# Kernel tuning notes

Hardware: AMD Instinct MI355X
Metric: run time of the kernel (lower is better)

## Reference

```python
import jax, jax.numpy as jnp
import numpy as np

EPS = 1e-12  # F.normalize default eps


def _sage_conv(x, src, dst, num_nodes, W_l, W_r, b):
    # mean-aggregate neighbor features: for each dst node, mean over x[src]
    agg = jax.ops.segment_sum(x[src], dst, num_segments=num_nodes)  # [N, d_in]
    cnt = jax.ops.segment_sum(jnp.ones((src.shape[0],), x.dtype), dst,
                              num_segments=num_nodes)
    mean = agg / jnp.maximum(cnt, 1.0)[:, None]
    # PyG SAGEConv: lin_l(aggregated) + bias + lin_r(root)
    return mean @ W_l + b + x @ W_r


def setup_inputs() -> dict:
    key = jax.random.key(0)
    ks = jax.random.split(key, 10)
    N, E, F_in = 50000, 400000, 128
    x = jax.random.normal(ks[0], (N, F_in), dtype=jnp.float32)
    edge_index = jax.random.randint(ks[1], (2, E), 0, N, dtype=jnp.int64)

    def lin(k, din, dout):
        s = 1.0 / np.sqrt(din)
        return jax.random.uniform(k, (din, dout), jnp.float32, -s, s)

    params = {
        "W1_l": lin(ks[2], F_in, 2048), "W1_r": lin(ks[3], F_in, 2048),
        "b1": jnp.zeros((2048,), jnp.float32),
        "W2_l": lin(ks[4], 2048, 2048), "W2_r": lin(ks[5], 2048, 2048),
        "b2": jnp.zeros((2048,), jnp.float32),
        "W3_l": lin(ks[6], 2048, 1024), "W3_r": lin(ks[7], 2048, 1024),
        "b3": jnp.zeros((1024,), jnp.float32),
    }
    return {"x": x, "unused": 0, "edge_index": edge_index, **params}


def reference(x, unused, edge_index,
              W1_l, W1_r, b1, W2_l, W2_r, b2, W3_l, W3_r, b3):
    del unused
    N = x.shape[0]
    src, dst = edge_index[0], edge_index[1]
    h = jax.nn.relu(_sage_conv(x, src, dst, N, W1_l, W1_r, b1))
    h = jax.nn.relu(_sage_conv(h, src, dst, N, W2_l, W2_r, b2))
    h = jax.nn.relu(_sage_conv(h, src, dst, N, W3_l, W3_r, b3))
    # F.normalize(dim=1): x / max(||x||_2, eps)
    norm = jnp.linalg.norm(h, axis=1, keepdims=True)
    return h / jnp.maximum(norm, EPS)
```

## Files before the change

### kernel.cpp

```cpp
#include <hip/hip_runtime.h>
#include <stdint.h>

#define NN 50000
#define EE 400000

typedef unsigned short u16;
typedef __attribute__((ext_vector_type(8))) short bf16x8;
typedef __attribute__((ext_vector_type(4))) float f32x4;
typedef __attribute__((address_space(3))) uint32_t lds_u32_t;
typedef __attribute__((address_space(1))) uint32_t glob_u32_t;

__device__ inline float bf2f(u16 u) {
  union { uint32_t i; float f; } x; x.i = ((uint32_t)u) << 16; return x.f;
}
__device__ inline u16 f2bf(float f) {
  union { float f; uint32_t i; } x; x.f = f;
  x.i += 0x7fffu + ((x.i >> 16) & 1u);
  return (u16)(x.i >> 16);
}
__device__ inline void gload_lds16(const void* g, void* l) {
  __builtin_amdgcn_global_load_lds((const glob_u32_t*)g, (lds_u32_t*)l, 16, 0, 0);
}

__global__ void detect_i64(const int* __restrict__ e, int* __restrict__ flag) {
  __shared__ int sh[256];
  int t = threadIdx.x;
  int v = 0;
  for (int i = t; i < 4096; i += 256) v |= e[2 * i + 1];
  sh[t] = v; __syncthreads();
  for (int s = 128; s > 0; s >>= 1) { if (t < s) sh[t] |= sh[t + s]; __syncthreads(); }
  if (t == 0) flag[0] = (sh[0] == 0) ? 1 : 0;
}

__global__ void conv_edges(const int* __restrict__ e, const int* __restrict__ flag,
                           int* __restrict__ src, int* __restrict__ dst) {
  int i = blockIdx.x * 256 + threadIdx.x;
  if (i >= EE) return;
  if (flag[0]) { src[i] = e[2 * i]; dst[i] = e[2 * (EE + i)]; }
  else         { src[i] = e[i];     dst[i] = e[EE + i]; }
}

__global__ void count_edges(const int* __restrict__ dst, int* __restrict__ cnt) {
  int i = blockIdx.x * 256 + threadIdx.x;
  if (i < EE) atomicAdd(&cnt[dst[i]], 1);
}

__global__ void scan_counts(const int* __restrict__ cnt, int* __restrict__ offs,
                            int* __restrict__ cursor) {
  __shared__ int sh[1024];
  __shared__ int carry_sh;
  int tid = threadIdx.x;
  if (tid == 0) carry_sh = 0;
  __syncthreads();
  int nChunks = (NN + 1023) / 1024;
  for (int c = 0; c < nChunks; ++c) {
    int idx = c * 1024 + tid;
    int v = (idx < NN) ? cnt[idx] : 0;
    sh[tid] = v; __syncthreads();
    for (int off = 1; off < 1024; off <<= 1) {
      int t = (tid >= off) ? sh[tid - off] : 0;
      __syncthreads();
      sh[tid] += t;
      __syncthreads();
    }
    int incl = sh[tid];
    int excl = incl - v + carry_sh;
    if (idx < NN) { offs[idx] = excl; cursor[idx] = excl; }
    __syncthreads();
    if (tid == 0) carry_sh += sh[1023];
    __syncthreads();
  }
}

__global__ void fill_buckets(const int* __restrict__ src, const int* __restrict__ dst,
                             int* __restrict__ cursor, int* __restrict__ bucket) {
  int i = blockIdx.x * 256 + threadIdx.x;
  if (i >= EE) return;
  int p = atomicAdd(&cursor[dst[i]], 1);
  bucket[p] = src[i];
}

__global__ void cvt_bf16(const float* __restrict__ in, u16* __restrict__ out, int n4) {
  int i = blockIdx.x * 256 + threadIdx.x;
  if (i >= n4) return;
  float4 v = ((const float4*)in)[i];
  u16 o[4] = { f2bf(v.x), f2bf(v.y), f2bf(v.z), f2bf(v.w) };
  uint2 pack;
  pack.x = (uint32_t)o[0] | ((uint32_t)o[1] << 16);
  pack.y = (uint32_t)o[2] | ((uint32_t)o[3] << 16);
  ((uint2*)out)[i] = pack;
}

__global__ void transposeW(const float* __restrict__ W, u16* __restrict__ Wt,
                           int K, int Nc) {
  __shared__ float tile[32][33];
  int n0 = blockIdx.x * 32, k0 = blockIdx.y * 32;
  int tx = threadIdx.x, ty = threadIdx.y;
  #pragma unroll
  for (int i = 0; i < 4; ++i)
    tile[ty + i * 8][tx] = W[(size_t)(k0 + ty + i * 8) * Nc + n0 + tx];
  __syncthreads();
  #pragma unroll
  for (int i = 0; i < 4; ++i)
    Wt[(size_t)(n0 + ty + i * 8) * K + k0 + tx] = f2bf(tile[tx][ty + i * 8]);
}

template<int D>
__global__ void agg_mean(const u16* __restrict__ h, const int* __restrict__ offs,
                         const int* __restrict__ cnt, const int* __restrict__ bucket,
                         u16* __restrict__ outp) {
  int node = blockIdx.x;
  int t = threadIdx.x;
  int base = t * 8;
  if (base >= D) return;
  int start = offs[node];
  int c = cnt[node];
  float acc[8];
  #pragma unroll
  for (int i = 0; i < 8; ++i) acc[i] = 0.f;
  for (int j = 0; j < c; ++j) {
    int s = bucket[start + j];
    uint4 q = *(const uint4*)(h + (size_t)s * D + base);
    acc[0] += bf2f((u16)(q.x & 0xffff)); acc[1] += bf2f((u16)(q.x >> 16));
    acc[2] += bf2f((u16)(q.y & 0xffff)); acc[3] += bf2f((u16)(q.y >> 16));
    acc[4] += bf2f((u16)(q.z & 0xffff)); acc[5] += bf2f((u16)(q.z >> 16));
    acc[6] += bf2f((u16)(q.w & 0xffff)); acc[7] += bf2f((u16)(q.w >> 16));
  }
  float inv = 1.0f / fmaxf((float)c, 1.0f);
  uint4 o;
  o.x = (uint32_t)f2bf(acc[0] * inv) | ((uint32_t)f2bf(acc[1] * inv) << 16);
  o.y = (uint32_t)f2bf(acc[2] * inv) | ((uint32_t)f2bf(acc[3] * inv) << 16);
  o.z = (uint32_t)f2bf(acc[4] * inv) | ((uint32_t)f2bf(acc[5] * inv) << 16);
  o.w = (uint32_t)f2bf(acc[6] * inv) | ((uint32_t)f2bf(acc[7] * inv) << 16);
  *(uint4*)(outp + (size_t)node * D + base) = o;
}


template<int K>
__device__ inline void stage_half(char* ldsX, const u16* __restrict__ G, int grow0,
                                  int k0, int h, int wave, int lrow8, int slot8,
                                  int clampR) {
  #pragma unroll
  for (int j = 0; j < 2; ++j) {
    const int lrow = h * 128 + j * 64 + wave * 8;
    int gr = grow0 + lrow + lrow8;
    gr = gr < clampR ? gr : clampR - 1;
    gload_lds16(G + (size_t)gr * K + k0 + slot8, ldsX + lrow * 128);
  }
}

#define LOAD_A(BASE, MH)                                                        \
  _Pragma("unroll") for (int mf = 0; mf < 4; ++mf) {                            \
    af[mf][0] = *(const bf16x8*)((BASE) + ((MH) * 128 + mf * 16) * 128 + kc0);  \
    af[mf][1] = *(const bf16x8*)((BASE) + ((MH) * 128 + mf * 16) * 128 + kc1);  \
  }
#define LOAD_B(DST, BASE, NH)                                                   \
  _Pragma("unroll") for (int nf = 0; nf < 2; ++nf) {                            \
    DST[nf][0] = *(const bf16x8*)((BASE) + ((NH) * 128 + nf * 16) * 128 + kc0); \
    DST[nf][1] = *(const bf16x8*)((BASE) + ((NH) * 128 + nf * 16) * 128 + kc1); \
  }
#define QUAD(MH, BREG, NH)                                                      \
  _Pragma("unroll") for (int mf = 0; mf < 4; ++mf)                              \
  _Pragma("unroll") for (int nf = 0; nf < 2; ++nf) {                            \
    acc[(MH)*4+mf][(NH)*2+nf] = __builtin_amdgcn_mfma_f32_16x16x32_bf16(        \
        af[mf][0], BREG[nf][0], acc[(MH)*4+mf][(NH)*2+nf], 0, 0, 0);            \
    acc[(MH)*4+mf][(NH)*2+nf] = __builtin_amdgcn_mfma_f32_16x16x32_bf16(        \
        af[mf][1], BREG[nf][1], acc[(MH)*4+mf][(NH)*2+nf], 0, 0, 0);            \
  }
#define PHASE_BAR()                                                             \
  __builtin_amdgcn_s_barrier();                                                 \
  __builtin_amdgcn_sched_barrier(0)

template<int K, bool OUT_F32>
__global__ __launch_bounds__(512, 2)
void gemm8ph(const u16* __restrict__ A1, const u16* __restrict__ A2,
             const u16* __restrict__ B1t, const u16* __restrict__ B2t,
             const float* __restrict__ bias, void* __restrict__ Cout,
             int M, int Nc, int tilesN) {
  __shared__ __align__(16) char lds[131072];
  constexpr int NTp = K / 64;
  constexpr int NT = 2 * NTp;

  const int nwg = gridDim.x;
  const int bid = blockIdx.x;
  const int wg = (bid & 7) * (nwg >> 3) + (bid >> 3);
  const int bx = wg % tilesN, by = wg / tilesN;
  const int rowBase = by * 256, colBase = bx * 256;

  const int tid = threadIdx.x;
  const int lane = tid & 63;
  const int wave = tid >> 6;
  const int wm = wave >> 2, wn = wave & 3;
  const int r = lane & 15, kg = lane >> 4;
  const int sw = (r & 7) << 4;
  const int kc0 = (kg * 16) ^ sw;
  const int kc1 = (64 + kg * 16) ^ sw;
  const int slot8 = ((lane & 7) ^ ((lane >> 3) & 7)) * 8;
  const int lrow8 = lane >> 3;

  char* const pA0 = lds + (wm * 64 + r) * 128;
  char* const pB0 = lds + 32768 + (wn * 32 + r) * 128;

  f32x4 acc[8][4];
  #pragma unroll
  for (int m = 0; m < 8; ++m)
    #pragma unroll
    for (int n = 0; n < 4; ++n) acc[m][n] = (f32x4){0.f, 0.f, 0.f, 0.f};

  bf16x8 af[4][2], b0[2][2], b1[2][2];

  stage_half<K>(lds,         A1,  rowBase, 0, 0, wave, lrow8, slot8, M);
  stage_half<K>(lds + 32768, B1t, colBase, 0, 0, wave, lrow8, slot8, Nc);
  stage_half<K>(lds + 32768, B1t, colBase, 0, 1, wave, lrow8, slot8, Nc);
  stage_half<K>(lds,         A1,  rowBase, 0, 1, wave, lrow8, slot8, M);
  asm volatile("s_waitcnt vmcnt(0)" ::: "memory");
  PHASE_BAR();
  LOAD_A(pA0, 0);
  LOAD_B(b0, pB0, 0);

  for (int t = 0; t < NT; ++t) {
    const int cur = t & 1;
    const char* cA = pA0 + cur * 65536;
    const char* cB = pB0 + cur * 65536;
    const char* nAr = pA0 + (cur ^ 1) * 65536;
    const char* nBr = pB0 + (cur ^ 1) * 65536;
    char* nA = lds + (cur ^ 1) * 65536;
    char* nB = nA + 32768;
    const int vt = t + 1;
    const u16* sA; const u16* sB; int sk0;
    if (vt >= NTp) { sA = A2; sB = B2t; sk0 = (vt - NTp) * 64; }
    else           { sA = A1; sB = B1t; sk0 = vt * 64; }

    if (vt < NT) {
      stage_half<K>(nA, sA, rowBase, sk0, 0, wave, lrow8, slot8, M);
      stage_half<K>(nB, sB, colBase, sk0, 0, wave, lrow8, slot8, Nc);
      stage_half<K>(nB, sB, colBase, sk0, 1, wave, lrow8, slot8, Nc);
      stage_half<K>(nA, sA, rowBase, sk0, 1, wave, lrow8, slot8, M);
    }
    __builtin_amdgcn_s_setprio(1);
    QUAD(0, b0, 0);
    __builtin_amdgcn_s_setprio(0);
    LOAD_B(b1, cB, 1);
    PHASE_BAR();

    __builtin_amdgcn_s_setprio(1);
    QUAD(0, b1, 1);
    __builtin_amdgcn_s_setprio(0);
    LOAD_A(cA, 1);
    PHASE_BAR();

    __builtin_amdgcn_s_setprio(1);
    QUAD(1, b1, 1);
    __builtin_amdgcn_s_setprio(0);
    asm volatile("s_waitcnt vmcnt(4)" ::: "memory");
    PHASE_BAR();

    __builtin_amdgcn_s_setprio(1);
    QUAD(1, b0, 0);
    __builtin_amdgcn_s_setprio(0);
    LOAD_A(nAr, 0);
    LOAD_B(b0, nBr, 0);
    asm volatile("s_waitcnt vmcnt(0)" ::: "memory");
    PHASE_BAR();
  }

  const int q = lane >> 4;
  #pragma unroll
  for (int m = 0; m < 8; ++m) {
    int row = rowBase + (m >> 2) * 128 + wm * 64 + (m & 3) * 16 + q * 4;
    #pragma unroll
    for (int n = 0; n < 4; ++n) {
      int col = colBase + (n >> 1) * 128 + wn * 32 + (n & 1) * 16 + r;
      float bv = bias[col];
      #pragma unroll
      for (int reg = 0; reg < 4; ++reg) {
        if (row + reg < M) {
          float v = acc[m][n][reg] + bv;
          v = fmaxf(v, 0.f);
          if constexpr (OUT_F32)
            ((float*)Cout)[(size_t)(row + reg) * Nc + col] = v;
          else
            ((u16*)Cout)[(size_t)(row + reg) * Nc + col] = f2bf(v);
        }
      }
    }
  }
}

__global__ void l2norm_rows(float* __restrict__ out) {
  int node = blockIdx.x;
  int t = threadIdx.x;
  float4* p = (float4*)(out + (size_t)node * 1024);
  float4 v = p[t];
  float ss = v.x * v.x + v.y * v.y + v.z * v.z + v.w * v.w;
  #pragma unroll
  for (int off = 32; off > 0; off >>= 1) ss += __shfl_down(ss, off);
  __shared__ float sw[4];
  int lane = t & 63, w = t >> 6;
  if (lane == 0) sw[w] = ss;
  __syncthreads();
  float total = sw[0] + sw[1] + sw[2] + sw[3];
  float scale = 1.0f / fmaxf(sqrtf(total), 1e-12f);
  v.x *= scale; v.y *= scale; v.z *= scale; v.w *= scale;
  p[t] = v;
}

extern "C" void kernel_launch(void* const* d_in, const int* in_sizes, int n_in,
                              void* d_out, int out_size, void* d_ws, size_t ws_size,
                              hipStream_t stream) {
  const float* x   = (const float*)d_in[0];
  const int*   eix = (const int*)d_in[2];
  const float* W1l = (const float*)d_in[3];
  const float* W1r = (const float*)d_in[4];
  const float* b1  = (const float*)d_in[5];
  const float* W2l = (const float*)d_in[6];
  const float* W2r = (const float*)d_in[7];
  const float* b2  = (const float*)d_in[8];
  const float* W3l = (const float*)d_in[9];
  const float* W3r = (const float*)d_in[10];
  const float* b3  = (const float*)d_in[11];

  char* ws = (char*)d_ws;
  size_t off = 0;
  auto alloc = [&](size_t bytes) -> char* {
    char* p = ws + off;
    off += (bytes + 255) & ~(size_t)255;
    return p;
  };
  int* flag   = (int*)alloc(4);
  int* srcA   = (int*)alloc((size_t)EE * 4);
  int* dstA   = (int*)alloc((size_t)EE * 4);
  int* bucket = (int*)alloc((size_t)EE * 4);
  int* cnt    = (int*)alloc((size_t)NN * 4);
  int* offs   = (int*)alloc((size_t)NN * 4);
  int* cursor = (int*)alloc((size_t)NN * 4);
  u16* xb     = (u16*)alloc((size_t)NN * 128 * 2);
  u16* mean1  = (u16*)alloc((size_t)NN * 128 * 2);
  u16* W1lT   = (u16*)alloc((size_t)2048 * 128 * 2);
  u16* W1rT   = (u16*)alloc((size_t)2048 * 128 * 2);
  u16* W2lT   = (u16*)alloc((size_t)2048 * 2048 * 2);
  u16* W2rT   = (u16*)alloc((size_t)2048 * 2048 * 2);
  u16* W3lT   = (u16*)alloc((size_t)1024 * 2048 * 2);
  u16* W3rT   = (u16*)alloc((size_t)1024 * 2048 * 2);
  u16* bufA   = (u16*)alloc((size_t)NN * 2048 * 2);
  u16* bufB   = (u16*)alloc((size_t)NN * 2048 * 2);
  u16* mean2  = (u16*)d_out;

  detect_i64<<<1, 256, 0, stream>>>(eix, flag);
  conv_edges<<<(EE + 255) / 256, 256, 0, stream>>>(eix, flag, srcA, dstA);

  hipMemsetAsync(cnt, 0, (size_t)NN * 4, stream);
  count_edges<<<(EE + 255) / 256, 256, 0, stream>>>(dstA, cnt);
  scan_counts<<<1, 1024, 0, stream>>>(cnt, offs, cursor);
  fill_buckets<<<(EE + 255) / 256, 256, 0, stream>>>(srcA, dstA, cursor, bucket);

  cvt_bf16<<<(NN * 128 / 4 + 255) / 256, 256, 0, stream>>>(x, xb, NN * 128 / 4);
  transposeW<<<dim3(2048 / 32, 128 / 32), dim3(32, 8), 0, stream>>>(W1l, W1lT, 128, 2048);
  transposeW<<<dim3(2048 / 32, 128 / 32), dim3(32, 8), 0, stream>>>(W1r, W1rT, 128, 2048);
  transposeW<<<dim3(2048 / 32, 2048 / 32), dim3(32, 8), 0, stream>>>(W2l, W2lT, 2048, 2048);
  transposeW<<<dim3(2048 / 32, 2048 / 32), dim3(32, 8), 0, stream>>>(W2r, W2rT, 2048, 2048);
  transposeW<<<dim3(1024 / 32, 2048 / 32), dim3(32, 8), 0, stream>>>(W3l, W3lT, 2048, 1024);
  transposeW<<<dim3(1024 / 32, 2048 / 32), dim3(32, 8), 0, stream>>>(W3r, W3rT, 2048, 1024);

  const int tilesM = (NN + 255) / 256;

  agg_mean<128><<<NN, 64, 0, stream>>>(xb, offs, cnt, bucket, mean1);
  gemm8ph<128, false><<<tilesM * 8, 512, 0, stream>>>(
      mean1, xb, W1lT, W1rT, b1, bufA, NN, 2048, 8);

  agg_mean<2048><<<NN, 256, 0, stream>>>(bufA, offs, cnt, bucket, mean2);
  gemm8ph<2048, false><<<tilesM * 8, 512, 0, stream>>>(
      mean2, bufA, W2lT, W2rT, b2, bufB, NN, 2048, 8);

  agg_mean<2048><<<NN, 256, 0, stream>>>(bufB, offs, cnt, bucket, bufA);
  gemm8ph<2048, true><<<tilesM * 4, 512, 0, stream>>>(
      bufA, bufB, W3lT, W3rT, b3, d_out, NN, 1024, 4);

  l2norm_rows<<<NN, 256, 0, stream>>>((float*)d_out);
}
```

Baseline: 2.350 ms.

## Restructure GEMM main loop into two-phase pipeline with split global staging

Reorganizes the 8-phase GEMM loop into two larger phases per k-tile. Each phase issues its LDS reads and half of the next tile's global-to-LDS staging up front, then runs two MFMA quads, with partial vmcnt waits instead of a full drain. The last tile is peeled out so the loop needs no conditional staging. This aims to cut barrier count and let global loads overlap more compute, at the cost of more live registers and more delicate wait-count correctness.

```diff
diff --git a/kernel.cpp b/kernel.cpp
--- a/kernel.cpp
+++ b/kernel.cpp
@@ -167,9 +167,12 @@
     acc[(MH)*4+mf][(NH)*2+nf] = __builtin_amdgcn_mfma_f32_16x16x32_bf16(        \
         af[mf][1], BREG[nf][1], acc[(MH)*4+mf][(NH)*2+nf], 0, 0, 0);            \
   }
-#define PHASE_BAR()                                                             \
-  __builtin_amdgcn_s_barrier();                                                 \
-  __builtin_amdgcn_sched_barrier(0)
+#define BAR() __builtin_amdgcn_s_barrier()
+#define LGKM0()                                                                 \
+  do {                                                                          \
+    asm volatile("s_waitcnt lgkmcnt(0)" ::: "memory");                          \
+    __builtin_amdgcn_sched_barrier(0);                                          \
+  } while (0)
 
 template<int K, bool OUT_F32>
 __global__ __launch_bounds__(512, 2)
@@ -213,17 +216,13 @@
   stage_half<K>(lds + 32768, B1t, colBase, 0, 0, wave, lrow8, slot8, Nc);
   stage_half<K>(lds + 32768, B1t, colBase, 0, 1, wave, lrow8, slot8, Nc);
   stage_half<K>(lds,         A1,  rowBase, 0, 1, wave, lrow8, slot8, M);
-  asm volatile("s_waitcnt vmcnt(0)" ::: "memory");
-  PHASE_BAR();
-  LOAD_A(pA0, 0);
-  LOAD_B(b0, pB0, 0);
-
-  for (int t = 0; t < NT; ++t) {
+  asm volatile("s_waitcnt vmcnt(2)" ::: "memory");
+  BAR();
+
+  for (int t = 0; t < NT - 1; ++t) {
     const int cur = t & 1;
     const char* cA = pA0 + cur * 65536;
     const char* cB = pB0 + cur * 65536;
-    const char* nAr = pA0 + (cur ^ 1) * 65536;
-    const char* nBr = pB0 + (cur ^ 1) * 65536;
     char* nA = lds + (cur ^ 1) * 65536;
     char* nB = nA + 32768;
     const int vt = t + 1;
@@ -231,37 +230,52 @@
     if (vt >= NTp) { sA = A2; sB = B2t; sk0 = (vt - NTp) * 64; }
     else           { sA = A1; sB = B1t; sk0 = vt * 64; }
 
-    if (vt < NT) {
-      stage_half<K>(nA, sA, rowBase, sk0, 0, wave, lrow8, slot8, M);
-      stage_half<K>(nB, sB, colBase, sk0, 0, wave, lrow8, slot8, Nc);
-      stage_half<K>(nB, sB, colBase, sk0, 1, wave, lrow8, slot8, Nc);
-      stage_half<K>(nA, sA, rowBase, sk0, 1, wave, lrow8, slot8, M);
-    }
+    LOAD_A(cA, 0); LOAD_B(b0, cB, 0); LOAD_B(b1, cB, 1);
+    stage_half<K>(nA, sA, rowBase, sk0, 0, wave, lrow8, slot8, M);
+    stage_half<K>(nB, sB, colBase, sk0, 0, wave, lrow8, slot8, Nc);
+    BAR();
+    LGKM0();
     __builtin_amdgcn_s_setprio(1);
     QUAD(0, b0, 0);
-    __builtin_amdgcn_s_setprio(0);
-    LOAD_B(b1, cB, 1);
-    PHASE_BAR();
-
-    __builtin_amdgcn_s_setprio(1);
     QUAD(0, b1, 1);
     __builtin_amdgcn_s_setprio(0);
+    asm volatile("s_waitcnt vmcnt(4)" ::: "memory");
+    BAR();
+
     LOAD_A(cA, 1);
-    PHASE_BAR();
-
+    stage_half<K>(nB, sB, colBase, sk0, 1, wave, lrow8, slot8, Nc);
+    stage_half<K>(nA, sA, rowBase, sk0, 1, wave, lrow8, slot8, M);
+    BAR();
+    LGKM0();
     __builtin_amdgcn_s_setprio(1);
     QUAD(1, b1, 1);
-    __builtin_amdgcn_s_setprio(0);
-    asm volatile("s_waitcnt vmcnt(4)" ::: "memory");
-    PHASE_BAR();
-
-    __builtin_amdgcn_s_setprio(1);
     QUAD(1, b0, 0);
     __builtin_amdgcn_s_setprio(0);
-    LOAD_A(nAr, 0);
-    LOAD_B(b0, nBr, 0);
+    asm volatile("s_waitcnt vmcnt(2)" ::: "memory");
+    BAR();
+  }
+
+  {
+    const int cur = (NT - 1) & 1;
+    const char* cA = pA0 + cur * 65536;
+    const char* cB = pB0 + cur * 65536;
+
+    LOAD_A(cA, 0); LOAD_B(b0, cB, 0); LOAD_B(b1, cB, 1);
+    BAR();
+    LGKM0();
+    __builtin_amdgcn_s_setprio(1);
+    QUAD(0, b0, 0);
+    QUAD(0, b1, 1);
+    __builtin_amdgcn_s_setprio(0);
     asm volatile("s_waitcnt vmcnt(0)" ::: "memory");
-    PHASE_BAR();
+    BAR();
+
+    LOAD_A(cA, 1);
+    LGKM0();
+    __builtin_amdgcn_s_setprio(1);
+    QUAD(1, b1, 1);
+    QUAD(1, b0, 0);
+    __builtin_amdgcn_s_setprio(0);
   }
 
   const int q = lane >> 4;
```

Measured after the change: 2.282 ms. -2.9%, faster.
